# Kernel tuning notes

Measured on AMD Instinct MI355X. Metric: run time of the kernel, lower is better.

The kernel has to match this reference:

```python
import jax, jax.numpy as jnp
import numpy as np

BITS = (2, 4, 8)
GROUP = 4
EPS = 1e-5


def _ste_round(x):
    return x + jax.lax.stop_gradient(jnp.round(x) - x)


def _quant_act(x, b):
    s = float(2 ** b - 1)
    return _ste_round(jnp.clip(x, 0.0, 1.0) * s) / s


def _quant_weight(w, mean, std, b):
    # normalize by (mean, std) of the gating-selected channels, then b-bit uniform quant on [-1, 1]
    wn = jnp.clip((w - mean) / (std + EPS), -1.0, 1.0)
    s = float(2 ** b - 1)
    u = _ste_round((wn + 1.0) * 0.5 * s) / s
    return 2.0 * u - 1.0


def _mixed_qconv(x, w, w_mean, w_std, w_logits, a_logits):
    # bitwidth-selectable conv: softmax mixture over quantized weights / activations
    pw = jax.nn.softmax(w_logits)
    pa = jax.nn.softmax(a_logits)
    w_mix = sum(pw[i] * _quant_weight(w, w_mean, w_std, b) for i, b in enumerate(BITS))
    x_mix = sum(pa[i] * _quant_act(x, b) for i, b in enumerate(BITS))
    return jax.lax.conv_general_dilated(
        x_mix, w_mix, window_strides=(1, 1), padding='SAME',
        dimension_numbers=('NCHW', 'OIHW', 'NCHW'))


def _bn(x, g, b, m, v):
    inv = jax.lax.rsqrt(v + EPS)
    return (x - m[None, :, None, None]) * (g * inv)[None, :, None, None] + b[None, :, None, None]


def _masked_mean_std(w, mask):
    # mean/std over gate-selected filter slices; torch uses .data -> stop_gradient, unbiased std
    m = jnp.broadcast_to(mask, w.shape)
    cnt = jnp.sum(m)
    mean = jnp.sum(w * m) / cnt
    var = jnp.sum(m * (w - mean) ** 2) / (cnt - 1.0)
    return jax.lax.stop_gradient(mean), jax.lax.stop_gradient(jnp.sqrt(var))


def _indicator(w1, thr):
    n, c, h, wk = w1.shape
    fw = w1.reshape(n // GROUP, GROUP * c * h * wk)
    nf = fw / jnp.max(jnp.abs(fw))
    norm = jnp.sum(jnp.abs(nf), axis=1) / (GROUP * c * h * wk)  # [n_choices]
    soft = jax.nn.sigmoid(norm - thr)
    hard = (norm > thr).astype(w1.dtype)
    return hard - jax.lax.stop_gradient(soft) + soft  # STE indicator


def setup_inputs() -> dict:
    key = jax.random.key(0)
    ks = jax.random.split(key, 10)
    B, C, H, W = 64, 256, 32, 32
    return {
        'x': jax.random.normal(ks[0], (B, C, H, W), jnp.float32),
        'w1': jax.random.normal(ks[1], (C, C, 3, 3), jnp.float32) * 0.05,
        'w2': jax.random.normal(ks[2], (C, C, 3, 3), jnp.float32) * 0.05,
        'bn1_gamma': jnp.ones((C,), jnp.float32),
        'bn1_beta': jnp.zeros((C,), jnp.float32),
        'bn1_mean': jax.random.normal(ks[3], (C,), jnp.float32) * 0.1,
        'bn1_var': jax.random.uniform(ks[4], (C,), jnp.float32, 0.5, 1.5),
        'bn2_gamma': jnp.ones((C,), jnp.float32),
        'bn2_beta': jnp.zeros((C,), jnp.float32),
        'bn2_mean': jax.random.normal(ks[5], (C,), jnp.float32) * 0.1,
        'bn2_var': jax.random.uniform(ks[6], (C,), jnp.float32, 0.5, 1.5),
        'threshold': jnp.zeros((1,), jnp.float32),
        'w_logits1': jax.random.normal(ks[7], (3,), jnp.float32) * 0.1,
        'a_logits1': jax.random.normal(ks[8], (3,), jnp.float32) * 0.1,
        'w_logits2': jax.random.normal(ks[9], (3,), jnp.float32) * 0.1,
        'a_logits2': jnp.zeros((3,), jnp.float32),
    }


def reference(x, w1, w2, bn1_gamma, bn1_beta, bn1_mean, bn1_var,
              bn2_gamma, bn2_beta, bn2_mean, bn2_var, threshold,
              w_logits1, a_logits1, w_logits2, a_logits2):
    thr = threshold[0]
    ind = _indicator(w1, thr)                       # [n_choices]
    ind_ch = jnp.repeat(ind, GROUP)                 # [out_plane]
    gate_mask = jax.lax.stop_gradient((ind_ch > 0).astype(x.dtype))

    # both_preact path
    residual = x
    h = jax.nn.relu(_bn(x, bn1_gamma, bn1_beta, bn1_mean, bn1_var))
    m1, s1 = _masked_mean_std(w1, gate_mask[:, None, None, None])
    h = _mixed_qconv(h, w1, m1, s1, w_logits1, a_logits1)
    h = jax.nn.relu(_bn(h, bn2_gamma, bn2_beta, bn2_mean, bn2_var))
    m2, s2 = _masked_mean_std(w2, gate_mask[None, :, None, None])
    h = h * ind_ch[None, :, None, None]             # differentiable channel gating
    h = _mixed_qconv(h, w2, m2, s2, w_logits2, a_logits2)
    return h + residual
```

## Files before the change

### kernel.cpp

```cpp
#include <hip/hip_runtime.h>
#include <stdint.h>

#define EPSF 1e-5f

typedef _Float16 h8_t __attribute__((ext_vector_type(8)));
typedef float f4_t __attribute__((ext_vector_type(4)));

#define BB 64
#define CC 256
#define HH 32
#define WW 32
#define HP 34
#define WP 34
#define PADIMG (HP*WP*CC)
#define PADTOT (BB*PADIMG)

#define S_GSUM   0
#define S_GMAX   64
#define S_W1S    128
#define S_W1Q    192
#define S_W2S    256
#define S_W2Q    320
#define S_PA2    384
#define S_INDCH  400
#define S_BN2SC  656
#define S_BN2SH  912

#define OFF_STATS 0
#define OFF_A1    8192
#define OFF_A2    (OFF_A1 + PADTOT*2)
#define OFF_W1T   (OFF_A2 + PADTOT*2)
#define OFF_W2T   (OFF_W1T + 9*CC*CC*2)

__device__ __forceinline__ void async_load16(void* lds, const void* g) {
  __builtin_amdgcn_global_load_lds(
      reinterpret_cast<uint32_t __attribute__((address_space(1)))*>((uintptr_t)g),
      reinterpret_cast<uint32_t __attribute__((address_space(3)))*>((uint32_t)(uintptr_t)lds),
      16, 0, 0);
}

#define WAITV(N) asm volatile("s_waitcnt vmcnt(" #N ")" ::: "memory")

__device__ __forceinline__ float wave_sum(float v) {
  for (int o = 32; o; o >>= 1) v += __shfl_down(v, o);
  return v;
}
__device__ __forceinline__ float wave_max(float v) {
  for (int o = 32; o; o >>= 1) v = fmaxf(v, __shfl_down(v, o));
  return v;
}

__device__ __forceinline__ void softmax3(const float* l, float* out) {
  float m = fmaxf(fmaxf(l[0], l[1]), l[2]);
  float e0 = expf(l[0] - m), e1 = expf(l[1] - m), e2 = expf(l[2] - m);
  float inv = 1.f / (e0 + e1 + e2);
  out[0] = e0 * inv; out[1] = e1 * inv; out[2] = e2 * inv;
}

__device__ __forceinline__ float qmix_act(float v, float p0, float p1, float p2) {
  float cl = fminf(fmaxf(v, 0.f), 1.f);
  return p0 * (rintf(cl * 3.f) / 3.f) + p1 * (rintf(cl * 15.f) / 15.f)
       + p2 * (rintf(cl * 255.f) / 255.f);
}

__global__ void k_stats(const float* __restrict__ w1, const float* __restrict__ w2,
                        float* stats) {
  __shared__ float red[4][4];
  int bid = blockIdx.x, t = threadIdx.x;
  int lane = t & 63, w = t >> 6;
  if (bid < 64) {
    const float* p = w1 + bid * 9216;
    float sa = 0.f, s = 0.f, q = 0.f, mx = 0.f;
    for (int i = t; i < 9216; i += 256) {
      float v = p[i];
      float a = fabsf(v);
      sa += a; s += v; q += v * v; mx = fmaxf(mx, a);
    }
    sa = wave_sum(sa); s = wave_sum(s); q = wave_sum(q); mx = wave_max(mx);
    if (lane == 0) { red[w][0] = sa; red[w][1] = s; red[w][2] = q; red[w][3] = mx; }
    __syncthreads();
    if (t == 0) {
      float a = 0, b = 0, c = 0, d = 0;
      for (int k = 0; k < 4; ++k) {
        a += red[k][0]; b += red[k][1]; c += red[k][2]; d = fmaxf(d, red[k][3]);
      }
      stats[S_GSUM + bid] = a;
      stats[S_W1S + bid] = b;
      stats[S_W1Q + bid] = c;
      stats[S_GMAX + bid] = d;
    }
  } else {
    int g = bid - 64;
    const float* p = w2 + (size_t)t * 2304 + g * 36;
    float s = 0.f, q = 0.f;
#pragma unroll
    for (int i = 0; i < 36; ++i) { float v = p[i]; s += v; q += v * v; }
    s = wave_sum(s); q = wave_sum(q);
    if (lane == 0) { red[w][0] = s; red[w][1] = q; }
    __syncthreads();
    if (t == 0) {
      float a = 0, b = 0;
      for (int k = 0; k < 4; ++k) { a += red[k][0]; b += red[k][1]; }
      stats[S_W2S + g] = a;
      stats[S_W2Q + g] = b;
    }
  }
}

#define WPS 264
#define APR_STRIDE 264
__global__ void k_fused(const float* __restrict__ w1, const float* __restrict__ w2,
                        const float* __restrict__ xin, const float* __restrict__ thr_p,
                        const float* __restrict__ bn1g, const float* __restrict__ bn1b,
                        const float* __restrict__ bn1m, const float* __restrict__ bn1v,
                        const float* __restrict__ bn2g, const float* __restrict__ bn2b,
                        const float* __restrict__ bn2m, const float* __restrict__ bn2v,
                        const float* __restrict__ wl1, const float* __restrict__ al1,
                        const float* __restrict__ wl2, const float* __restrict__ al2,
                        float* __restrict__ stats,
                        _Float16* __restrict__ wt1, _Float16* __restrict__ wt2,
                        _Float16* __restrict__ a1, _Float16* __restrict__ a2) {
  int bid = blockIdx.x, t = threadIdx.x;

  if (bid == 0) {
    __shared__ float sind[64];
    if (t < 64) {
      float thr = thr_p[0];
      float mx = wave_max(stats[S_GMAX + t]);
      mx = __shfl(mx, 0);
      float norm = stats[S_GSUM + t] / mx / 9216.0f;
      float soft = 1.f / (1.f + expf(-(norm - thr)));
      float hard = (norm > thr) ? 1.f : 0.f;
      sind[t] = (hard - soft) + soft;
    }
    __syncthreads();
    stats[S_INDCH + t] = sind[t >> 2];
    float sc2 = bn2g[t] * (1.f / sqrtf(bn2v[t] + EPSF));
    stats[S_BN2SC + t] = sc2;
    stats[S_BN2SH + t] = bn2b[t] - bn2m[t] * sc2;
    if (t == 0) softmax3(al2, stats + S_PA2);
    return;
  }

  if (bid <= 64) {
    __shared__ __attribute__((aligned(16))) _Float16 lds[8 * 9 * WPS];
    __shared__ float sM, sSD, sP[3];
    int which = (bid - 1) >> 5;
    int o0 = ((bid - 1) & 31) * 8;
    if (t < 64) {
      float thr = thr_p[0];
      float mx = wave_max(stats[S_GMAX + t]);
      mx = __shfl(mx, 0);
      float norm = stats[S_GSUM + t] / mx / 9216.0f;
      float soft = 1.f / (1.f + expf(-(norm - thr)));
      float hard = (norm > thr) ? 1.f : 0.f;
      float iv = (hard - soft) + soft;
      float gate = (iv > 0.f) ? 1.f : 0.f;
      float ng = wave_sum(gate);
      float s = wave_sum(gate * stats[(which ? S_W2S : S_W1S) + t]);
      float q = wave_sum(gate * stats[(which ? S_W2Q : S_W1Q) + t]);
      if (t == 0) {
        float cnt = ng * 9216.0f;
        float m = s / cnt;
        float v = (q - cnt * m * m) / (cnt - 1.0f);
        sM = m; sSD = sqrtf(fmaxf(v, 0.f));
        softmax3(which ? wl2 : wl1, sP);
      }
    }
    __syncthreads();
    const float* w = (which ? w2 : w1) + (size_t)o0 * 2304;
    float mean = sM, sd = sSD + EPSF;
    float p0 = sP[0], p1 = sP[1], p2 = sP[2];
#pragma unroll
    for (int it = 0; it < 72; ++it) {
      int f = it * 256 + t;
      float v = w[f];
      float wn = fminf(fmaxf((v - mean) / sd, -1.f), 1.f);
      float u0 = rintf((wn + 1.f) * 0.5f * 3.f) / 3.f;
      float u1 = rintf((wn + 1.f) * 0.5f * 15.f) / 15.f;
      float u2 = rintf((wn + 1.f) * 0.5f * 255.f) / 255.f;
      float mix = p0 * (2.f * u0 - 1.f) + p1 * (2.f * u1 - 1.f) + p2 * (2.f * u2 - 1.f);
      int ff = f / 2304;
      int rem = f - 2304 * ff;
      int ci = rem / 9;
      int e = rem - 9 * ci;
      lds[(ff * 9 + e) * WPS + ci] = (_Float16)mix;
    }
    __syncthreads();
    _Float16* dstW = (which ? wt2 : wt1);
#pragma unroll
    for (int it = 0; it < 9; ++it) {
      int qid = it * 256 + t;
      int ff = qid & 7, pair = qid >> 3;
      int e = pair >> 5, cq = pair & 31;
      int kc2 = cq >> 3, kk2 = (cq >> 2) & 1, ks2 = cq & 3;
      size_t off = (size_t)((((kc2 * 9 + e) * 2 + kk2) * 4 + ks2)) * 2048
                 + (size_t)(o0 + ff) * 8;
      *(h8_t*)(dstW + off) = *(const h8_t*)(lds + (ff * 9 + e) * WPS + cq * 8);
    }
    return;
  }

  int ab = bid - 65;
  if (ab >= BB * HH) {
    int b = ab - BB * HH;
    _Float16* img = (b >= BB ? a2 : a1) + (size_t)(b & 63) * PADIMG;
    uint64_t* u = (uint64_t*)img;
#pragma unroll
    for (int it = 0; it < 17; ++it) {
      int idx = it * 256 + t;
      int r33 = (idx >= 2176);
      u[(size_t)(r33 ? 33 * WP * 64 : 0) + (idx - (r33 ? 2176 : 0))] = 0ull;
    }
#pragma unroll
    for (int it = 0; it < 16; ++it) {
      int idx = it * 256 + t;
      int p = idx >> 6;
      int y = 1 + (p >> 1), x = (p & 1) ? 33 : 0;
      u[(size_t)(y * WP + x) * 64 + (idx & 63)] = 0ull;
    }
    return;
  }

  __shared__ __attribute__((aligned(16))) _Float16 lds[32 * APR_STRIDE];
  __shared__ float sBsc[256], sBsh[256], sPa[3];
  {
    float sc1 = bn1g[t] * (1.f / sqrtf(bn1v[t] + EPSF));
    sBsc[t] = sc1;
    sBsh[t] = bn1b[t] - bn1m[t] * sc1;
    if (t == 0) softmax3(al1, sPa);
  }
  __syncthreads();
  int n = ab >> 5, y = ab & 31;
  int x4 = (t & 7) * 4, c0 = t >> 3;
  float pa0 = sPa[0], pa1 = sPa[1], pa2 = sPa[2];
#pragma unroll
  for (int it = 0; it < 8; ++it) {
    int c = it * 32 + c0;
    const float* src = xin + ((size_t)(n * CC + c) * HH + y) * WW + x4;
    float4 v = *(const float4*)src;
    float sc = sBsc[c], sh = sBsh[c];
#pragma unroll
    for (int k = 0; k < 4; ++k) {
      float q = qmix_act((&v.x)[k] * sc + sh, pa0, pa1, pa2);
      lds[(x4 + k) * APR_STRIDE + c] = (_Float16)q;
    }
  }
  __syncthreads();
  _Float16* orow = a1 + ((size_t)(n * HP + (y + 1)) * WP + 1) * CC;
#pragma unroll
  for (int it = 0; it < 4; ++it) {
    int qid = it * 256 + t;
    int xx = qid >> 5, c8 = (qid & 31) * 8;
    *(h8_t*)(orow + xx * CC + c8) = *(const h8_t*)(lds + xx * APR_STRIDE + c8);
  }
}

template <bool SW>
__global__ __launch_bounds__(256) void k_conv(
    const _Float16* __restrict__ act,
    const _Float16* __restrict__ wts,
    const float* __restrict__ stats,
    _Float16* __restrict__ a2out,
    const float* __restrict__ resid,
    float* __restrict__ out) {
  __shared__ __attribute__((aligned(16))) _Float16 AT[224 * 64];
  const int tid = threadIdx.x;
  const int lane = tid & 63, wid = tid >> 6;
  const int xcd = blockIdx.x & 7;
  const int j = blockIdx.x >> 3;
  const int blk_co = j >> 6;
  const int blk_m = xcd * 64 + (j & 63);

  const int n0 = blk_m >> 3;
  const int y0 = (blk_m & 7) * 4;
  const _Float16* actbase = act + (size_t)(n0 * HP + y0) * WP * CC;

  const int wr = wid >> 1, wc = wid & 1;
  const int mrow = (SW ? wc : wr) * 64;
  const int wrow = (SW ? wr : wc) * 64;
  const int ksl = lane >> 4;

  const int base34 = (mrow >> 5) * 34 + (lane & 15);

  const _Float16* wptr =
      wts + (size_t)(ksl * 2048 + (blk_co * 128 + wrow + (lane & 15)) * 8);

  f4_t acc[4][4];
  const f4_t z4 = {0.f, 0.f, 0.f, 0.f};
#pragma unroll
  for (int i = 0; i < 4; ++i)
#pragma unroll
    for (int j2 = 0; j2 < 4; ++j2) acc[i][j2] = z4;

  auto stageA = [&](int kcn) {
    const int kb = kcn * 64;
#pragma unroll
    for (int it = 0; it < 7; ++it) {
      int l = it * 256 + tid;
      int tr = l >> 3, gg = l & 7;
      int yl = tr / 34, px = tr - yl * 34;
      async_load16(AT + l * 8,
                   actbase + ((size_t)yl * WP + px) * CC + kb + ((gg ^ (tr & 7)) * 8));
    }
  };

  h8_t fwA[4], fwB[4];
  auto loadW = [&](h8_t* dst) {
#pragma unroll
    for (int i = 0; i < 4; ++i)
      dst[i] = *(const h8_t*)(wptr + i * 128);
    wptr += 8192;
  };

  stageA(0);
  loadW(fwA);
  loadW(fwB);
  WAITV(8);
  __builtin_amdgcn_sched_barrier(0);
  __builtin_amdgcn_s_barrier();

#pragma unroll 1
  for (int kc = 0; kc < 4; ++kc) {
#pragma unroll 1
    for (int e = 0; e < 9; ++e) {
      const int d3 = (e * 43) >> 7;
      const int de = e + 31 * d3;
      const int t0 = base34 + de;
      {
        h8_t fa[4];
#pragma unroll
        for (int i = 0; i < 4; ++i) {
          const int tr = t0 + (i == 0 ? 0 : i == 1 ? 16 : i == 2 ? 34 : 50);
          fa[i] = *(const h8_t*)(AT + ((tr * 64 + ((ksl ^ (tr & 7)) * 8))));
        }
        __builtin_amdgcn_s_setprio(1);
#pragma unroll
        for (int i = 0; i < 4; ++i)
#pragma unroll
          for (int j2 = 0; j2 < 4; ++j2)
            acc[i][j2] = __builtin_amdgcn_mfma_f32_16x16x32_f16(
                SW ? fwA[i] : fa[i], SW ? fa[j2] : fwA[j2], acc[i][j2], 0, 0, 0);
        __builtin_amdgcn_s_setprio(0);
      }
      if (e < 8) loadW(fwA);
      {
        h8_t fa[4];
#pragma unroll
        for (int i = 0; i < 4; ++i) {
          const int tr = t0 + (i == 0 ? 0 : i == 1 ? 16 : i == 2 ? 34 : 50);
          fa[i] = *(const h8_t*)(AT + ((tr * 64 + ((ksl ^ (tr & 7)) * 8)) ^ 32));
        }
        __builtin_amdgcn_s_setprio(1);
#pragma unroll
        for (int i = 0; i < 4; ++i)
#pragma unroll
          for (int j2 = 0; j2 < 4; ++j2)
            acc[i][j2] = __builtin_amdgcn_mfma_f32_16x16x32_f16(
                SW ? fwB[i] : fa[i], SW ? fa[j2] : fwB[j2], acc[i][j2], 0, 0, 0);
        __builtin_amdgcn_s_setprio(0);
      }
      if (e < 8) loadW(fwB);
    }
    if (kc < 3) {
      asm volatile("s_waitcnt lgkmcnt(0)" ::: "memory");
      __builtin_amdgcn_sched_barrier(0);
      __builtin_amdgcn_s_barrier();
      __builtin_amdgcn_sched_barrier(0);
      stageA(kc + 1);
      loadW(fwA);
      loadW(fwB);
      WAITV(8);
      __builtin_amdgcn_sched_barrier(0);
      __builtin_amdgcn_s_barrier();
    }
  }

  const int quad = lane >> 4;
  const int cq = lane & 15;
  if (!SW) {
    const float pa0 = stats[S_PA2], pa1 = stats[S_PA2 + 1], pa2 = stats[S_PA2 + 2];
#pragma unroll
    for (int j2 = 0; j2 < 4; ++j2) {
      const int co = blk_co * 128 + wc * 64 + j2 * 16 + cq;
      const float sc = stats[S_BN2SC + co];
      const float sh = stats[S_BN2SH + co];
      const float ic = stats[S_INDCH + co];
#pragma unroll
      for (int i = 0; i < 4; ++i) {
        const int mbase = blk_m * 128 + wr * 64 + i * 16 + quad * 4;
#pragma unroll
        for (int rg = 0; rg < 4; ++rg) {
          const int m = mbase + rg;
          const int n = m >> 10, y = (m >> 5) & 31, x = m & 31;
          float h = fmaxf(acc[i][j2][rg] * sc + sh, 0.f) * ic;
          float q = qmix_act(h, pa0, pa1, pa2);
          a2out[((size_t)(n * HP + y + 1) * WP + (x + 1)) * CC + co] = (_Float16)q;
        }
      }
    }
  } else {
#pragma unroll
    for (int j2 = 0; j2 < 4; ++j2) {
      const int m = blk_m * 128 + wc * 64 + j2 * 16 + cq;
      const int n = m >> 10, y = (m >> 5) & 31, x = m & 31;
#pragma unroll
      for (int i = 0; i < 4; ++i) {
        const int cobase = blk_co * 128 + wr * 64 + i * 16 + quad * 4;
#pragma unroll
        for (int rg = 0; rg < 4; ++rg) {
          const int co = cobase + rg;
          const int idx = ((n * CC + co) << 10) + (y << 5) + x;
          out[idx] = acc[i][j2][rg] + resid[idx];
        }
      }
    }
  }
}

extern "C" void kernel_launch(void* const* d_in, const int* in_sizes, int n_in,
                              void* d_out, int out_size, void* d_ws, size_t ws_size,
                              hipStream_t stream) {
  const float* x    = (const float*)d_in[0];
  const float* w1   = (const float*)d_in[1];
  const float* w2   = (const float*)d_in[2];
  const float* bn1g = (const float*)d_in[3];
  const float* bn1b = (const float*)d_in[4];
  const float* bn1m = (const float*)d_in[5];
  const float* bn1v = (const float*)d_in[6];
  const float* bn2g = (const float*)d_in[7];
  const float* bn2b = (const float*)d_in[8];
  const float* bn2m = (const float*)d_in[9];
  const float* bn2v = (const float*)d_in[10];
  const float* thr  = (const float*)d_in[11];
  const float* wl1  = (const float*)d_in[12];
  const float* al1  = (const float*)d_in[13];
  const float* wl2  = (const float*)d_in[14];
  const float* al2  = (const float*)d_in[15];

  char* ws = (char*)d_ws;
  float* stats = (float*)(ws + OFF_STATS);
  _Float16* a1 = (_Float16*)(ws + OFF_A1);
  _Float16* a2 = (_Float16*)(ws + OFF_A2);
  _Float16* wt1 = (_Float16*)(ws + OFF_W1T);
  _Float16* wt2 = (_Float16*)(ws + OFF_W2T);
  float* out = (float*)d_out;

  k_stats<<<128, 256, 0, stream>>>(w1, w2, stats);
  k_fused<<<1 + 64 + BB * HH + 128, 256, 0, stream>>>(
      w1, w2, x, thr, bn1g, bn1b, bn1m, bn1v, bn2g, bn2b, bn2m, bn2v,
      wl1, al1, wl2, al2, stats, wt1, wt2, a1, a2);
  k_conv<false><<<1024, 256, 0, stream>>>(a1, wt1, stats, a2, nullptr, nullptr);
  k_conv<true><<<1024, 256, 0, stream>>>(a2, wt2, stats, nullptr, x, out);
}
```

Baseline: 349.2 us.

## Stage conv1 epilogue through LDS for vectorized stores; split prep kernel

The first conv's epilogue now writes quantized fp16 activations into an LDS tile (AT) in two halves, then stores them to the padded NHWC buffer as 16-byte vectors. Previously each lane wrote scattered 2-byte values. The fused prep kernel is also split into separate activation-prep and weight-prep launches. The aim is better-coalesced global writes for a2, at the cost of extra barriers, LDS traffic and one more kernel launch.

```diff
diff --git a/kernel.cpp b/kernel.cpp
--- a/kernel.cpp
+++ b/kernel.cpp
@@ -108,18 +108,14 @@
 }
 
 #define WPS 264
-#define APR_STRIDE 264
-__global__ void k_fused(const float* __restrict__ w1, const float* __restrict__ w2,
-                        const float* __restrict__ xin, const float* __restrict__ thr_p,
-                        const float* __restrict__ bn1g, const float* __restrict__ bn1b,
-                        const float* __restrict__ bn1m, const float* __restrict__ bn1v,
+__global__ void k_wprep(const float* __restrict__ w1, const float* __restrict__ w2,
+                        const float* __restrict__ thr_p,
                         const float* __restrict__ bn2g, const float* __restrict__ bn2b,
                         const float* __restrict__ bn2m, const float* __restrict__ bn2v,
-                        const float* __restrict__ wl1, const float* __restrict__ al1,
-                        const float* __restrict__ wl2, const float* __restrict__ al2,
+                        const float* __restrict__ wl1, const float* __restrict__ wl2,
+                        const float* __restrict__ al2,
                         float* __restrict__ stats,
-                        _Float16* __restrict__ wt1, _Float16* __restrict__ wt2,
-                        _Float16* __restrict__ a1, _Float16* __restrict__ a2) {
+                        _Float16* __restrict__ wt1, _Float16* __restrict__ wt2) {
   int bid = blockIdx.x, t = threadIdx.x;
 
   if (bid == 0) {
@@ -142,68 +138,73 @@
     return;
   }
 
-  if (bid <= 64) {
-    __shared__ __attribute__((aligned(16))) _Float16 lds[8 * 9 * WPS];
-    __shared__ float sM, sSD, sP[3];
-    int which = (bid - 1) >> 5;
-    int o0 = ((bid - 1) & 31) * 8;
-    if (t < 64) {
-      float thr = thr_p[0];
-      float mx = wave_max(stats[S_GMAX + t]);
-      mx = __shfl(mx, 0);
-      float norm = stats[S_GSUM + t] / mx / 9216.0f;
-      float soft = 1.f / (1.f + expf(-(norm - thr)));
-      float hard = (norm > thr) ? 1.f : 0.f;
-      float iv = (hard - soft) + soft;
-      float gate = (iv > 0.f) ? 1.f : 0.f;
-      float ng = wave_sum(gate);
-      float s = wave_sum(gate * stats[(which ? S_W2S : S_W1S) + t]);
-      float q = wave_sum(gate * stats[(which ? S_W2Q : S_W1Q) + t]);
-      if (t == 0) {
-        float cnt = ng * 9216.0f;
-        float m = s / cnt;
-        float v = (q - cnt * m * m) / (cnt - 1.0f);
-        sM = m; sSD = sqrtf(fmaxf(v, 0.f));
-        softmax3(which ? wl2 : wl1, sP);
-      }
-    }
-    __syncthreads();
-    const float* w = (which ? w2 : w1) + (size_t)o0 * 2304;
-    float mean = sM, sd = sSD + EPSF;
-    float p0 = sP[0], p1 = sP[1], p2 = sP[2];
-#pragma unroll
-    for (int it = 0; it < 72; ++it) {
-      int f = it * 256 + t;
-      float v = w[f];
-      float wn = fminf(fmaxf((v - mean) / sd, -1.f), 1.f);
-      float u0 = rintf((wn + 1.f) * 0.5f * 3.f) / 3.f;
-      float u1 = rintf((wn + 1.f) * 0.5f * 15.f) / 15.f;
-      float u2 = rintf((wn + 1.f) * 0.5f * 255.f) / 255.f;
-      float mix = p0 * (2.f * u0 - 1.f) + p1 * (2.f * u1 - 1.f) + p2 * (2.f * u2 - 1.f);
-      int ff = f / 2304;
-      int rem = f - 2304 * ff;
-      int ci = rem / 9;
-      int e = rem - 9 * ci;
-      lds[(ff * 9 + e) * WPS + ci] = (_Float16)mix;
-    }
-    __syncthreads();
-    _Float16* dstW = (which ? wt2 : wt1);
-#pragma unroll
-    for (int it = 0; it < 9; ++it) {
-      int qid = it * 256 + t;
-      int ff = qid & 7, pair = qid >> 3;
-      int e = pair >> 5, cq = pair & 31;
-      int kc2 = cq >> 3, kk2 = (cq >> 2) & 1, ks2 = cq & 3;
-      size_t off = (size_t)((((kc2 * 9 + e) * 2 + kk2) * 4 + ks2)) * 2048
-                 + (size_t)(o0 + ff) * 8;
-      *(h8_t*)(dstW + off) = *(const h8_t*)(lds + (ff * 9 + e) * WPS + cq * 8);
-    }
-    return;
-  }
-
-  int ab = bid - 65;
-  if (ab >= BB * HH) {
-    int b = ab - BB * HH;
+  __shared__ __attribute__((aligned(16))) _Float16 lds[8 * 9 * WPS];
+  __shared__ float sM, sSD, sP[3];
+  int which = (bid - 1) >> 5;
+  int o0 = ((bid - 1) & 31) * 8;
+  if (t < 64) {
+    float thr = thr_p[0];
+    float mx = wave_max(stats[S_GMAX + t]);
+    mx = __shfl(mx, 0);
+    float norm = stats[S_GSUM + t] / mx / 9216.0f;
+    float soft = 1.f / (1.f + expf(-(norm - thr)));
+    float hard = (norm > thr) ? 1.f : 0.f;
+    float iv = (hard - soft) + soft;
+    float gate = (iv > 0.f) ? 1.f : 0.f;
+    float ng = wave_sum(gate);
+    float s = wave_sum(gate * stats[(which ? S_W2S : S_W1S) + t]);
+    float q = wave_sum(gate * stats[(which ? S_W2Q : S_W1Q) + t]);
+    if (t == 0) {
+      float cnt = ng * 9216.0f;
+      float m = s / cnt;
+      float v = (q - cnt * m * m) / (cnt - 1.0f);
+      sM = m; sSD = sqrtf(fmaxf(v, 0.f));
+      softmax3(which ? wl2 : wl1, sP);
+    }
+  }
+  __syncthreads();
+  const float* w = (which ? w2 : w1) + (size_t)o0 * 2304;
+  float mean = sM, sd = sSD + EPSF;
+  float p0 = sP[0], p1 = sP[1], p2 = sP[2];
+#pragma unroll
+  for (int it = 0; it < 72; ++it) {
+    int f = it * 256 + t;
+    float v = w[f];
+    float wn = fminf(fmaxf((v - mean) / sd, -1.f), 1.f);
+    float u0 = rintf((wn + 1.f) * 0.5f * 3.f) / 3.f;
+    float u1 = rintf((wn + 1.f) * 0.5f * 15.f) / 15.f;
+    float u2 = rintf((wn + 1.f) * 0.5f * 255.f) / 255.f;
+    float mix = p0 * (2.f * u0 - 1.f) + p1 * (2.f * u1 - 1.f) + p2 * (2.f * u2 - 1.f);
+    int ff = f / 2304;
+    int rem = f - 2304 * ff;
+    int ci = rem / 9;
+    int e = rem - 9 * ci;
+    lds[(ff * 9 + e) * WPS + ci] = (_Float16)mix;
+  }
+  __syncthreads();
+  _Float16* dstW = (which ? wt2 : wt1);
+#pragma unroll
+  for (int it = 0; it < 9; ++it) {
+    int qid = it * 256 + t;
+    int ff = qid & 7, pair = qid >> 3;
+    int e = pair >> 5, cq = pair & 31;
+    int kc2 = cq >> 3, kk2 = (cq >> 2) & 1, ks2 = cq & 3;
+    size_t off = (size_t)((((kc2 * 9 + e) * 2 + kk2) * 4 + ks2)) * 2048
+               + (size_t)(o0 + ff) * 8;
+    *(h8_t*)(dstW + off) = *(const h8_t*)(lds + (ff * 9 + e) * WPS + cq * 8);
+  }
+}
+
+#define APR_STRIDE 264
+__global__ void k_aprep(const float* __restrict__ xin,
+                        const float* __restrict__ bn1g, const float* __restrict__ bn1b,
+                        const float* __restrict__ bn1m, const float* __restrict__ bn1v,
+                        const float* __restrict__ al1,
+                        _Float16* __restrict__ a1, _Float16* __restrict__ a2) {
+  int bid = blockIdx.x, t = threadIdx.x;
+
+  if (bid >= BB * HH) {
+    int b = bid - BB * HH;
     _Float16* img = (b >= BB ? a2 : a1) + (size_t)(b & 63) * PADIMG;
     uint64_t* u = (uint64_t*)img;
 #pragma unroll
@@ -231,7 +232,7 @@
     if (t == 0) softmax3(al1, sPa);
   }
   __syncthreads();
-  int n = ab >> 5, y = ab & 31;
+  int n = bid >> 5, y = bid & 31;
   int x4 = (t & 7) * 4, c0 = t >> 3;
   float pa0 = sPa[0], pa1 = sPa[1], pa2 = sPa[2];
 #pragma unroll
@@ -380,24 +381,40 @@
   const int cq = lane & 15;
   if (!SW) {
     const float pa0 = stats[S_PA2], pa1 = stats[S_PA2 + 1], pa2 = stats[S_PA2 + 2];
-#pragma unroll
-    for (int j2 = 0; j2 < 4; ++j2) {
-      const int co = blk_co * 128 + wc * 64 + j2 * 16 + cq;
-      const float sc = stats[S_BN2SC + co];
-      const float sh = stats[S_BN2SH + co];
-      const float ic = stats[S_INDCH + co];
-#pragma unroll
-      for (int i = 0; i < 4; ++i) {
-        const int mbase = blk_m * 128 + wr * 64 + i * 16 + quad * 4;
-#pragma unroll
-        for (int rg = 0; rg < 4; ++rg) {
-          const int m = mbase + rg;
-          const int n = m >> 10, y = (m >> 5) & 31, x = m & 31;
-          float h = fmaxf(acc[i][j2][rg] * sc + sh, 0.f) * ic;
-          float q = qmix_act(h, pa0, pa1, pa2);
-          a2out[((size_t)(n * HP + y + 1) * WP + (x + 1)) * CC + co] = (_Float16)q;
+    asm volatile("s_waitcnt lgkmcnt(0)" ::: "memory");
+    __builtin_amdgcn_s_barrier();
+#pragma unroll
+    for (int h = 0; h < 2; ++h) {
+      if (wr == h) {
+#pragma unroll
+        for (int j2 = 0; j2 < 4; ++j2) {
+          const int coidx = wc * 64 + j2 * 16 + cq;
+          const int co = blk_co * 128 + coidx;
+          const float sc = stats[S_BN2SC + co];
+          const float sh = stats[S_BN2SH + co];
+          const float ic = stats[S_INDCH + co];
+#pragma unroll
+          for (int i = 0; i < 4; ++i) {
+#pragma unroll
+            for (int rg = 0; rg < 4; ++rg) {
+              const int px = i * 16 + quad * 4 + rg;
+              float v = fmaxf(acc[i][j2][rg] * sc + sh, 0.f) * ic;
+              AT[px * 132 + coidx] = (_Float16)qmix_act(v, pa0, pa1, pa2);
+            }
+          }
         }
       }
+      __syncthreads();
+#pragma unroll
+      for (int it = 0; it < 4; ++it) {
+        const int qid = it * 256 + tid;
+        const int px = qid >> 4, c8 = (qid & 15) * 8;
+        const int m = blk_m * 128 + h * 64 + px;
+        const int n = m >> 10, y = (m >> 5) & 31, x = m & 31;
+        *(h8_t*)(a2out + ((size_t)(n * HP + y + 1) * WP + (x + 1)) * CC
+                 + blk_co * 128 + c8) = *(const h8_t*)(AT + px * 132 + c8);
+      }
+      __syncthreads();
     }
   } else {
 #pragma unroll
@@ -447,9 +464,9 @@
   float* out = (float*)d_out;
 
   k_stats<<<128, 256, 0, stream>>>(w1, w2, stats);
-  k_fused<<<1 + 64 + BB * HH + 128, 256, 0, stream>>>(
-      w1, w2, x, thr, bn1g, bn1b, bn1m, bn1v, bn2g, bn2b, bn2m, bn2v,
-      wl1, al1, wl2, al2, stats, wt1, wt2, a1, a2);
+  k_aprep<<<BB * HH + 128, 256, 0, stream>>>(x, bn1g, bn1b, bn1m, bn1v, al1, a1, a2);
+  k_wprep<<<65, 256, 0, stream>>>(w1, w2, thr, bn2g, bn2b, bn2m, bn2v,
+                                  wl1, wl2, al2, stats, wt1, wt2);
   k_conv<false><<<1024, 256, 0, stream>>>(a1, wt1, stats, a2, nullptr, nullptr);
   k_conv<true><<<1024, 256, 0, stream>>>(a2, wt2, stats, nullptr, x, out);
 }
```

Result: slower. 368.6 us (+5.6%).
